# Performance work log

Hardware: AMD Instinct MI355X
Metric: run time of the kernel (lower is better)

The kernel has to match this reference:

```python
import jax, jax.numpy as jnp
import numpy as np

N_NODES = 50000
N_EDGES = 800000
IN_F = 64
HID = 64
N_GRAPHS = 500
N_OUT = 2


def _glorot(key, shape):
    fan_in, fan_out = shape[1], shape[0]
    lim = float(np.sqrt(6.0 / (fan_in + fan_out)))
    return jax.random.uniform(key, shape, jnp.float32, -lim, lim)


def setup_inputs() -> dict:
    key = jax.random.key(0)
    ks = jax.random.split(key, 16)
    x = jax.random.normal(ks[0], (N_NODES, IN_F), jnp.float32)
    edge_index = jax.random.randint(ks[1], (2, N_EDGES), 0, N_NODES, jnp.int64)
    batch = jnp.sort(jax.random.randint(ks[2], (N_NODES,), 0, N_GRAPHS, jnp.int64))
    inp = {"x": x, "edge_index": edge_index, "batch": batch}
    # GraphConv params: out = lin_rel(aggr_add(x_j)) + lin_root(x); lin_rel has bias.
    dims = [(IN_F, HID), (HID, HID), (HID, HID)]
    for i, (din, dout) in enumerate(dims, start=1):
        inp[f"Wrel{i}"] = _glorot(ks[2 * i + 1], (dout, din))
        inp[f"brel{i}"] = jnp.zeros((dout,), jnp.float32)
        inp[f"Wroot{i}"] = _glorot(ks[2 * i + 2], (dout, din))
    inp["Wlin"] = _glorot(ks[10], (N_OUT, HID))
    inp["blin"] = jnp.zeros((N_OUT,), jnp.float32)
    return inp


def _graph_conv(x, src, dst, Wrel, brel, Wroot):
    # aggregate neighbor features (sum over incoming edges), then linear
    agg = jnp.zeros_like(x).at[dst].add(x[src])  # [N, F]
    return agg @ Wrel.T + brel + x @ Wroot.T


def reference(x, edge_index, batch,
              Wrel1, brel1, Wroot1,
              Wrel2, brel2, Wroot2,
              Wrel3, brel3, Wroot3,
              Wlin, blin):
    src, dst = edge_index[0], edge_index[1]
    h = jax.nn.relu(_graph_conv(x, src, dst, Wrel1, brel1, Wroot1))
    h = jax.nn.relu(_graph_conv(h, src, dst, Wrel2, brel2, Wroot2))
    h = _graph_conv(h, src, dst, Wrel3, brel3, Wroot3)
    # global mean pool over graphs
    sums = jax.ops.segment_sum(h, batch, num_segments=N_GRAPHS)
    cnt = jax.ops.segment_sum(jnp.ones((h.shape[0],), h.dtype), batch, num_segments=N_GRAPHS)
    pooled = sums / jnp.maximum(cnt, 1.0)[:, None]
    # dropout is identity in eval mode
    return pooled @ Wlin.T + blin
```

## Files before the change

kernel.cpp:

```cpp
#include <hip/hip_runtime.h>
#include <hip/hip_bf16.h>

#define N_NODES 50000
#define N_EDGES 800000
#define F 64
#define N_GRAPHS 500
#define NW ((N_NODES + 63) / 64)
#define PADW 68
#define FILL_PASSES 4
#define FILL_RANGE ((N_NODES + FILL_PASSES - 1) / FILL_PASSES)

__global__ __launch_bounds__(256) void hist_kernel(
    const int* __restrict__ edge, int* __restrict__ deg)
{
    int e = blockIdx.x * 256 + threadIdx.x;
    if (e < N_EDGES) atomicAdd(&deg[edge[N_EDGES + e]], 1);
}

__global__ __launch_bounds__(256) void wavesum_kernel(
    const int* __restrict__ deg, int* __restrict__ partial)
{
    int w = (blockIdx.x * 256 + threadIdx.x) >> 6;
    int lane = threadIdx.x & 63;
    if (w >= NW) return;
    int i = w * 64 + lane;
    int v = (i < N_NODES) ? deg[i] : 0;
#pragma unroll
    for (int d = 32; d > 0; d >>= 1) v += __shfl_xor(v, d);
    if (lane == 0) partial[w] = v;
}

__global__ __launch_bounds__(1024) void scanp_kernel(int* __restrict__ partial)
{
    __shared__ int ws[16];
    int t = threadIdx.x, lane = t & 63, wv = t >> 6;
    int v = (t < NW) ? partial[t] : 0;
    int incl = v;
#pragma unroll
    for (int d = 1; d < 64; d <<= 1) { int u = __shfl_up(incl, d); if (lane >= d) incl += u; }
    if (lane == 63) ws[wv] = incl;
    __syncthreads();
    if (wv == 0 && lane < 16) {
        int s = ws[lane];
#pragma unroll
        for (int d = 1; d < 16; d <<= 1) { int u = __shfl_up(s, d); if (lane >= d) s += u; }
        ws[lane] = s;
    }
    __syncthreads();
    int base = wv ? ws[wv - 1] : 0;
    if (t < NW) partial[t] = base + incl - v;
    if (t == 0) partial[NW] = ws[15];
}

__global__ __launch_bounds__(256) void offsets_kernel(
    const int* __restrict__ deg, const int* __restrict__ partial,
    int* __restrict__ off, int* __restrict__ cursor)
{
    int w = (blockIdx.x * 256 + threadIdx.x) >> 6;
    int lane = threadIdx.x & 63;
    if (w >= NW) return;
    int i = w * 64 + lane;
    int v = (i < N_NODES) ? deg[i] : 0;
    int incl = v;
#pragma unroll
    for (int d = 1; d < 64; d <<= 1) { int u = __shfl_up(incl, d); if (lane >= d) incl += u; }
    int excl = partial[w] + incl - v;
    if (i < N_NODES) { off[i] = excl; cursor[i] = excl; }
    if (w == 0 && lane == 0) off[N_NODES] = partial[NW];
}

__global__ __launch_bounds__(256) void fill_kernel(
    const int* __restrict__ edge, int* __restrict__ cursor, int* __restrict__ csr_src, int lo)
{
    int e = blockIdx.x * 256 + threadIdx.x;
    if (e < N_EDGES) {
        int dst = edge[N_EDGES + e];
        if (dst >= lo && dst < lo + FILL_RANGE) {
            int slot = atomicAdd(&cursor[dst], 1);
            csr_src[slot] = edge[e];
        }
    }
}

__global__ __launch_bounds__(256) void gather_kernel(
    const float* __restrict__ xin, const int* __restrict__ off,
    const int* __restrict__ csr_src, float* __restrict__ agg)
{
    int hw = (blockIdx.x * 256 + threadIdx.x) >> 5;
    if (hw >= N_NODES) return;
    int hl = threadIdx.x & 31;
    int g = hl >> 4;
    int q = (hl & 15) << 2;

    int beg = off[hw], end = off[hw + 1];
    float4 A0 = make_float4(0.f, 0.f, 0.f, 0.f);
    float4 A1 = A0, A2 = A0, A3 = A0, A4 = A0, A5 = A0, A6 = A0, A7 = A0;

    for (int base = beg; base < end; base += 16) {
#define GSTEP(K, ACC) { int e = base + g + 2 * (K); if (e < end) { \
        const float4 v = *reinterpret_cast<const float4*>(xin + (size_t)csr_src[e] * F + q); \
        ACC.x += v.x; ACC.y += v.y; ACC.z += v.z; ACC.w += v.w; } }
        GSTEP(0, A0) GSTEP(1, A1) GSTEP(2, A2) GSTEP(3, A3)
        GSTEP(4, A4) GSTEP(5, A5) GSTEP(6, A6) GSTEP(7, A7)
#undef GSTEP
    }
    float4 s;
    s.x = ((A0.x + A1.x) + (A2.x + A3.x)) + ((A4.x + A5.x) + (A6.x + A7.x));
    s.y = ((A0.y + A1.y) + (A2.y + A3.y)) + ((A4.y + A5.y) + (A6.y + A7.y));
    s.z = ((A0.z + A1.z) + (A2.z + A3.z)) + ((A4.z + A5.z) + (A6.z + A7.z));
    s.w = ((A0.w + A1.w) + (A2.w + A3.w)) + ((A4.w + A5.w) + (A6.w + A7.w));
    s.x += __shfl_xor(s.x, 16);
    s.y += __shfl_xor(s.y, 16);
    s.z += __shfl_xor(s.z, 16);
    s.w += __shfl_xor(s.w, 16);
    if (hl < 16)
        *reinterpret_cast<float4*>(agg + (size_t)hw * F + q) = s;
}

__global__ __launch_bounds__(256) void gemm_kernel(
    const float* __restrict__ agg, const float* __restrict__ xin,
    const float* __restrict__ Wrel, const float* __restrict__ brel,
    const float* __restrict__ Wroot, float* __restrict__ out, int do_relu)
{
    __shared__ float sA[64 * PADW];
    __shared__ float sX[64 * PADW];
    __shared__ float sWrel[64 * 64];
    __shared__ float sWroot[64 * 64];

    int tid = threadIdx.x;
    int n0 = blockIdx.x * 64;

    for (int i = tid; i < 64 * 16; i += 256) {
        int row = i >> 4, c4 = (i & 15) << 2;
        int node = n0 + row;
        float4 va = make_float4(0.f, 0.f, 0.f, 0.f), vx = va;
        if (node < N_NODES) {
            va = *reinterpret_cast<const float4*>(agg + (size_t)node * F + c4);
            vx = *reinterpret_cast<const float4*>(xin + (size_t)node * F + c4);
        }
        *reinterpret_cast<float4*>(sA + row * PADW + c4) = va;
        *reinterpret_cast<float4*>(sX + row * PADW + c4) = vx;
    }
    for (int i = tid; i < 64 * 16; i += 256) {
        int idx = i << 2;
        *reinterpret_cast<float4*>(sWrel + idx)  = *reinterpret_cast<const float4*>(Wrel + idx);
        *reinterpret_cast<float4*>(sWroot + idx) = *reinterpret_cast<const float4*>(Wroot + idx);
    }
    __syncthreads();

    int lane = tid & 63;
    int ob = __builtin_amdgcn_readfirstlane((tid >> 6) * 16);
    int n = n0 + lane;

    float acc[16];
#pragma unroll
    for (int j = 0; j < 16; ++j) acc[j] = brel[ob + j];

#pragma unroll
    for (int half = 0; half < 2; ++half) {
        const float* __restrict__ sW = half ? sWroot : sWrel;
        const float* __restrict__ s  = half ? sX : sA;
#pragma unroll
        for (int kc = 0; kc < F; kc += 4) {
            float4 a = *reinterpret_cast<const float4*>(s + lane * PADW + kc);
#pragma unroll
            for (int j = 0; j < 16; ++j) {
                float4 wv = *reinterpret_cast<const float4*>(sW + (ob + j) * F + kc);
                acc[j] += a.x * wv.x + a.y * wv.y + a.z * wv.z + a.w * wv.w;
            }
        }
    }
    if (do_relu) {
#pragma unroll
        for (int j = 0; j < 16; ++j) acc[j] = fmaxf(acc[j], 0.f);
    }
    if (n < N_NODES) {
#pragma unroll
        for (int j = 0; j < 16; j += 4)
            *reinterpret_cast<float4*>(out + (size_t)n * F + ob + j) =
                make_float4(acc[j], acc[j + 1], acc[j + 2], acc[j + 3]);
    }
}

__global__ __launch_bounds__(256) void pool_head_kernel(
    const float* __restrict__ h,
    const int* __restrict__ batch,
    const float* __restrict__ Wlin,
    const float* __restrict__ blin,
    float* __restrict__ out)
{
    __shared__ float psum[4][F];
    __shared__ float pooled[F];
    int g = blockIdx.x;
    int tid = threadIdx.x, wave = tid >> 6, lane = tid & 63;

    int lo = 0, hi = N_NODES;
    while (lo < hi) { int mid = (lo + hi) >> 1; if (batch[mid] < g) lo = mid + 1; else hi = mid; }
    int s = lo;
    hi = N_NODES;
    while (lo < hi) { int mid = (lo + hi) >> 1; if (batch[mid] < g + 1) lo = mid + 1; else hi = mid; }
    int e = lo;

    float acc = 0.f;
    for (int n = s + wave; n < e; n += 4) acc += h[n * F + lane];
    psum[wave][lane] = acc;
    __syncthreads();
    if (wave == 0) {
        float p = psum[0][lane] + psum[1][lane] + psum[2][lane] + psum[3][lane];
        float c = (float)(e - s);
        pooled[lane] = p / fmaxf(c, 1.0f);
    }
    __syncthreads();
    if (tid < 2) {
        float acc2 = 0.f;
#pragma unroll
        for (int k = 0; k < F; ++k) acc2 += pooled[k] * Wlin[tid * F + k];
        out[g * 2 + tid] = acc2 + blin[tid];
    }
}

extern "C" void kernel_launch(void* const* d_in, const int* in_sizes, int n_in,
                              void* d_out, int out_size, void* d_ws, size_t ws_size,
                              hipStream_t stream) {
    const float* x     = (const float*)d_in[0];
    const int*   edge  = (const int*)d_in[1];
    const int*   batch = (const int*)d_in[2];
    const float* Wrel1 = (const float*)d_in[3];
    const float* brel1 = (const float*)d_in[4];
    const float* Wroot1= (const float*)d_in[5];
    const float* Wrel2 = (const float*)d_in[6];
    const float* brel2 = (const float*)d_in[7];
    const float* Wroot2= (const float*)d_in[8];
    const float* Wrel3 = (const float*)d_in[9];
    const float* brel3 = (const float*)d_in[10];
    const float* Wroot3= (const float*)d_in[11];
    const float* Wlin  = (const float*)d_in[12];
    const float* blin  = (const float*)d_in[13];
    float* out = (float*)d_out;

    char* ws = (char*)d_ws;
    size_t p = 0;
    int* deg     = (int*)(ws + p); p += (size_t)N_NODES * 4;
    int* off     = (int*)(ws + p); p += (size_t)(N_NODES + 1) * 4;
    int* cursor  = (int*)(ws + p); p += (size_t)N_NODES * 4;
    int* partial = (int*)(ws + p); p += (size_t)(NW + 1) * 4;
    p = (p + 255) & ~(size_t)255;
    int* csr_src = (int*)(ws + p); p += (size_t)N_EDGES * 4;
    p = (p + 255) & ~(size_t)255;
    float* agg   = (float*)(ws + p); p += (size_t)N_NODES * F * 4;
    float* hA    = (float*)(ws + p); p += (size_t)N_NODES * F * 4;
    float* hB    = (float*)(ws + p); p += (size_t)N_NODES * F * 4;

    dim3 blk(256);
    const int edgeBlocks = (N_EDGES + 255) / 256;
    const int gatherBlocks = (N_NODES * 32 + 255) / 256;
    const int segBlocks = (NW + 3) / 4;

    hipMemsetAsync(deg, 0, (size_t)N_NODES * 4, stream);
    hist_kernel<<<edgeBlocks, blk, 0, stream>>>(edge, deg);
    wavesum_kernel<<<segBlocks, blk, 0, stream>>>(deg, partial);
    scanp_kernel<<<1, 1024, 0, stream>>>(partial);
    offsets_kernel<<<segBlocks, blk, 0, stream>>>(deg, partial, off, cursor);
    for (int pass = 0; pass < FILL_PASSES; ++pass)
        fill_kernel<<<edgeBlocks, blk, 0, stream>>>(edge, cursor, csr_src, pass * FILL_RANGE);

    gather_kernel<<<gatherBlocks, blk, 0, stream>>>(x, off, csr_src, agg);
    gemm_kernel<<<NW, blk, 0, stream>>>(agg, x, Wrel1, brel1, Wroot1, hA, 1);

    gather_kernel<<<gatherBlocks, blk, 0, stream>>>(hA, off, csr_src, agg);
    gemm_kernel<<<NW, blk, 0, stream>>>(agg, hA, Wrel2, brel2, Wroot2, hB, 1);

    gather_kernel<<<gatherBlocks, blk, 0, stream>>>(hB, off, csr_src, agg);
    gemm_kernel<<<NW, blk, 0, stream>>>(agg, hB, Wrel3, brel3, Wroot3, hA, 0);

    pool_head_kernel<<<N_GRAPHS, blk, 0, stream>>>(hA, batch, Wlin, blin, out);
}
```

Measured before the change: 399.3 us.

## Restructure GraphConv GEMM into 4x4 register-tiled outer product with transposed LDS

The dense GEMM now stores both the activation tiles (agg and x concatenated along K) and the weight matrices transposed in shared memory, each with a padded stride. Each thread computes a 4x4 output tile as an outer product over K=128. The previous version had each thread compute one node by 16 outputs with dot products, reading weights from LDS once per output. The new scheme is meant to cut LDS traffic per FMA and improve the FMA-to-load ratio. The cost is scalar transposing stores during staging, which may cause LDS bank conflicts, and row-strided float4 output stores.

Measured after the change: 360.7 us. -9.6%, faster.

```diff
diff --git a/kernel.cpp b/kernel.cpp
--- a/kernel.cpp
+++ b/kernel.cpp
@@ -6,7 +6,7 @@
 #define F 64
 #define N_GRAPHS 500
 #define NW ((N_NODES + 63) / 64)
-#define PADW 68
+#define PADT 68
 #define FILL_PASSES 4
 #define FILL_RANGE ((N_NODES + FILL_PASSES - 1) / FILL_PASSES)
 
@@ -122,63 +122,83 @@
     const float* __restrict__ Wrel, const float* __restrict__ brel,
     const float* __restrict__ Wroot, float* __restrict__ out, int do_relu)
 {
-    __shared__ float sA[64 * PADW];
-    __shared__ float sX[64 * PADW];
-    __shared__ float sWrel[64 * 64];
-    __shared__ float sWroot[64 * 64];
+    __shared__ float sAX[128 * PADT];
+    __shared__ float sW[128 * PADT];
 
     int tid = threadIdx.x;
     int n0 = blockIdx.x * 64;
 
     for (int i = tid; i < 64 * 16; i += 256) {
-        int row = i >> 4, c4 = (i & 15) << 2;
+        int row = i >> 4;
+        int c4 = (i & 15) << 2;
         int node = n0 + row;
         float4 va = make_float4(0.f, 0.f, 0.f, 0.f), vx = va;
         if (node < N_NODES) {
             va = *reinterpret_cast<const float4*>(agg + (size_t)node * F + c4);
             vx = *reinterpret_cast<const float4*>(xin + (size_t)node * F + c4);
         }
-        *reinterpret_cast<float4*>(sA + row * PADW + c4) = va;
-        *reinterpret_cast<float4*>(sX + row * PADW + c4) = vx;
-    }
-    for (int i = tid; i < 64 * 16; i += 256) {
-        int idx = i << 2;
-        *reinterpret_cast<float4*>(sWrel + idx)  = *reinterpret_cast<const float4*>(Wrel + idx);
-        *reinterpret_cast<float4*>(sWroot + idx) = *reinterpret_cast<const float4*>(Wroot + idx);
-    }
-    __syncthreads();
-
-    int lane = tid & 63;
-    int ob = __builtin_amdgcn_readfirstlane((tid >> 6) * 16);
-    int n = n0 + lane;
-
-    float acc[16];
-#pragma unroll
-    for (int j = 0; j < 16; ++j) acc[j] = brel[ob + j];
-
-#pragma unroll
-    for (int half = 0; half < 2; ++half) {
-        const float* __restrict__ sW = half ? sWroot : sWrel;
-        const float* __restrict__ s  = half ? sX : sA;
-#pragma unroll
-        for (int kc = 0; kc < F; kc += 4) {
-            float4 a = *reinterpret_cast<const float4*>(s + lane * PADW + kc);
-#pragma unroll
-            for (int j = 0; j < 16; ++j) {
-                float4 wv = *reinterpret_cast<const float4*>(sW + (ob + j) * F + kc);
-                acc[j] += a.x * wv.x + a.y * wv.y + a.z * wv.z + a.w * wv.w;
-            }
-        }
-    }
+        float4 wr = *reinterpret_cast<const float4*>(Wrel + row * F + c4);
+        float4 wo = *reinterpret_cast<const float4*>(Wroot + row * F + c4);
+        sAX[(c4 + 0) * PADT + row] = va.x;
+        sAX[(c4 + 1) * PADT + row] = va.y;
+        sAX[(c4 + 2) * PADT + row] = va.z;
+        sAX[(c4 + 3) * PADT + row] = va.w;
+        sAX[(64 + c4 + 0) * PADT + row] = vx.x;
+        sAX[(64 + c4 + 1) * PADT + row] = vx.y;
+        sAX[(64 + c4 + 2) * PADT + row] = vx.z;
+        sAX[(64 + c4 + 3) * PADT + row] = vx.w;
+        sW[(c4 + 0) * PADT + row] = wr.x;
+        sW[(c4 + 1) * PADT + row] = wr.y;
+        sW[(c4 + 2) * PADT + row] = wr.z;
+        sW[(c4 + 3) * PADT + row] = wr.w;
+        sW[(64 + c4 + 0) * PADT + row] = wo.x;
+        sW[(64 + c4 + 1) * PADT + row] = wo.y;
+        sW[(64 + c4 + 2) * PADT + row] = wo.z;
+        sW[(64 + c4 + 3) * PADT + row] = wo.w;
+    }
+    __syncthreads();
+
+    int tm = tid & 15, tn = tid >> 4;
+    const float* pA = sAX + tm * 4;
+    const float* pW = sW + tn * 4;
+
+    float acc[4][4];
+#pragma unroll
+    for (int i = 0; i < 4; ++i) {
+        float4 b = *reinterpret_cast<const float4*>(brel + tn * 4);
+        acc[i][0] = b.x; acc[i][1] = b.y; acc[i][2] = b.z; acc[i][3] = b.w;
+    }
+
+    for (int kk = 0; kk < 128; kk += 4) {
+        float4 a0 = *reinterpret_cast<const float4*>(pA + (kk + 0) * PADT);
+        float4 a1 = *reinterpret_cast<const float4*>(pA + (kk + 1) * PADT);
+        float4 a2 = *reinterpret_cast<const float4*>(pA + (kk + 2) * PADT);
+        float4 a3 = *reinterpret_cast<const float4*>(pA + (kk + 3) * PADT);
+        float4 w0 = *reinterpret_cast<const float4*>(pW + (kk + 0) * PADT);
+        float4 w1 = *reinterpret_cast<const float4*>(pW + (kk + 1) * PADT);
+        float4 w2 = *reinterpret_cast<const float4*>(pW + (kk + 2) * PADT);
+        float4 w3 = *reinterpret_cast<const float4*>(pW + (kk + 3) * PADT);
+#define FMA4(AV, WV) { \
+        acc[0][0] += AV.x * WV.x; acc[0][1] += AV.x * WV.y; acc[0][2] += AV.x * WV.z; acc[0][3] += AV.x * WV.w; \
+        acc[1][0] += AV.y * WV.x; acc[1][1] += AV.y * WV.y; acc[1][2] += AV.y * WV.z; acc[1][3] += AV.y * WV.w; \
+        acc[2][0] += AV.z * WV.x; acc[2][1] += AV.z * WV.y; acc[2][2] += AV.z * WV.z; acc[2][3] += AV.z * WV.w; \
+        acc[3][0] += AV.w * WV.x; acc[3][1] += AV.w * WV.y; acc[3][2] += AV.w * WV.z; acc[3][3] += AV.w * WV.w; }
+        FMA4(a0, w0) FMA4(a1, w1) FMA4(a2, w2) FMA4(a3, w3)
+#undef FMA4
+    }
+
     if (do_relu) {
 #pragma unroll
-        for (int j = 0; j < 16; ++j) acc[j] = fmaxf(acc[j], 0.f);
-    }
-    if (n < N_NODES) {
-#pragma unroll
-        for (int j = 0; j < 16; j += 4)
-            *reinterpret_cast<float4*>(out + (size_t)n * F + ob + j) =
-                make_float4(acc[j], acc[j + 1], acc[j + 2], acc[j + 3]);
+        for (int i = 0; i < 4; ++i)
+#pragma unroll
+            for (int j = 0; j < 4; ++j) acc[i][j] = fmaxf(acc[i][j], 0.f);
+    }
+#pragma unroll
+    for (int i = 0; i < 4; ++i) {
+        int n = n0 + tm * 4 + i;
+        if (n < N_NODES)
+            *reinterpret_cast<float4*>(out + (size_t)n * F + tn * 4) =
+                make_float4(acc[i][0], acc[i][1], acc[i][2], acc[i][3]);
     }
 }
 
```
